# Kernel tuning notes

Hardware: AMD Instinct MI355X
Metric: run time of the kernel (lower is better)

## Reference

```python
import jax, jax.numpy as jnp
import numpy as np

B, S, D = 4, 512, 512


def setup_inputs() -> dict:
    key = jax.random.key(0)
    k0, k1, k2 = jax.random.split(key, 3)
    x = jax.random.normal(k0, (B, S, D), jnp.float32)
    W1 = jax.random.normal(k1, (D, D // 2), jnp.float32) / np.sqrt(D).astype(np.float32)
    b1 = jnp.zeros((D // 2,), jnp.float32)
    W2 = jax.random.normal(k2, (D // 2, 1), jnp.float32) / np.sqrt(D // 2).astype(np.float32)
    b2 = jnp.zeros((1,), jnp.float32)
    # deterministic ragged durations in the module's ~10-30 frame range
    durations = jnp.broadcast_to(8 + (jnp.arange(S, dtype=jnp.int32) % 32), (B, S))
    total_length = int(np.asarray(durations).sum())  # 48128, static
    return dict(x=x, W1=W1, b1=b1, W2=W2, b2=b2, durations=durations,
                total_length=total_length)


def reference(x, W1, b1, W2, b2, durations, total_length):
    # --- duration-predictor MLP (Linear -> ReLU -> Linear -> Softplus) ---
    h = jax.nn.relu(jnp.einsum('bsd,df->bsf', x, W1) + b1)
    dur_mlp = jax.nn.softplus(jnp.einsum('bsf,fo->bso', h, W2) + b2)[..., 0]  # [B,S]

    # --- length regulation: gather + linear interpolation ---
    # torch code uses durations of batch row 0 for all batch elements, and
    # allocates total_length = sum over the WHOLE batch (trailing zeros kept).
    dur0 = durations[0].astype(jnp.int32)          # [S]
    csum = jnp.cumsum(dur0)                         # [S], csum[-1] = used length L
    L = csum[-1]
    t = jnp.arange(total_length, dtype=jnp.int32)   # [T]
    tok = jnp.searchsorted(csum, t, side='right')   # token index per output frame
    valid = t < L
    ic = jnp.minimum(tok, S - 1)
    j = t - (csum[ic] - dur0[ic])                   # offset within token's frames
    # last token: pure repeat (alpha=0); others: lerp toward x[:, i+1]
    alpha = jnp.where(ic == S - 1, 0.0,
                      j.astype(x.dtype) / dur0[ic].astype(x.dtype))  # [T]
    left = x[:, ic]                                 # [B,T,D]
    right = x[:, jnp.minimum(ic + 1, S - 1)]        # [B,T,D]
    a = alpha[None, :, None]
    expanded = (1.0 - a) * left + a * right
    expanded = jnp.where(valid[None, :, None], expanded, 0.0)
    return expanded, dur_mlp
```

## Files before the change

kernel.cpp:

```cpp
#include <hip/hip_runtime.h>
#include <math.h>

#define Bn 4
#define Sn 512
#define Dn 512
#define Fn 256
#define RROWS 8

struct Ent { float alpha; int ic; };

typedef float v4f __attribute__((ext_vector_type(4)));

__global__ __launch_bounds__(512) void prep_kernel(const int* __restrict__ dur,
                                                   Ent* __restrict__ tab, int T) {
    __shared__ int csum[Sn];
    int tid = threadIdx.x;
    csum[tid] = dur[tid];
    __syncthreads();
    #pragma unroll
    for (int off = 1; off < Sn; off <<= 1) {
        int add = (tid >= off) ? csum[tid - off] : 0;
        __syncthreads();
        csum[tid] += add;
        __syncthreads();
    }
    int L = csum[Sn - 1];
    int t = blockIdx.x * Sn + tid;
    if (t >= T) return;
    Ent e;
    if (t >= L) {
        e.alpha = 0.f; e.ic = -1;
    } else {
        int lo = 0, hi = Sn;
        while (lo < hi) {
            int mid = (lo + hi) >> 1;
            if (csum[mid] <= t) lo = mid + 1; else hi = mid;
        }
        int ic = lo;
        int start = ic ? csum[ic - 1] : 0;
        int d = csum[ic] - start;
        e.ic = ic;
        e.alpha = (ic == Sn - 1) ? 0.f : (float)(t - start) / (float)d;
    }
    tab[t] = e;
}

__global__ __launch_bounds__(256) void mlp_kernel(const float* __restrict__ x,
                                                  const float* __restrict__ W1,
                                                  const float* __restrict__ b1,
                                                  const float* __restrict__ W2,
                                                  const float* __restrict__ b2,
                                                  float* __restrict__ out_dur) {
    __shared__ float xs[RROWS][Dn];
    __shared__ float red[4][RROWS];
    int f = threadIdx.x;
    int r0 = blockIdx.x * RROWS;

    const float4* src = (const float4*)(x + (size_t)r0 * Dn);
    float4* dst = (float4*)(&xs[0][0]);
    for (int i = f; i < RROWS * Dn / 4; i += 256) dst[i] = src[i];
    __syncthreads();

    float acc[RROWS];
    #pragma unroll
    for (int r = 0; r < RROWS; r++) acc[r] = 0.f;

    for (int k = 0; k < Dn; k += 4) {
        float w0 = W1[(k + 0) * Fn + f];
        float w1 = W1[(k + 1) * Fn + f];
        float w2 = W1[(k + 2) * Fn + f];
        float w3 = W1[(k + 3) * Fn + f];
        #pragma unroll
        for (int r = 0; r < RROWS; r++) {
            float4 xv = *(const float4*)&xs[r][k];
            acc[r] += xv.x * w0 + xv.y * w1 + xv.z * w2 + xv.w * w3;
        }
    }

    float bb = b1[f], wf = W2[f];
    float p[RROWS];
    #pragma unroll
    for (int r = 0; r < RROWS; r++) {
        float h = acc[r] + bb;
        h = h > 0.f ? h : 0.f;
        p[r] = h * wf;
    }

    int lane = f & 63, wv = f >> 6;
    #pragma unroll
    for (int r = 0; r < RROWS; r++) {
        float v = p[r];
        #pragma unroll
        for (int off = 32; off > 0; off >>= 1) v += __shfl_down(v, off, 64);
        if (lane == 0) red[wv][r] = v;
    }
    __syncthreads();
    if (f < RROWS) {
        float z = red[0][f] + red[1][f] + red[2][f] + red[3][f] + b2[0];
        float sp = fmaxf(z, 0.f) + log1pf(expf(-fabsf(z)));
        out_dur[r0 + f] = sp;
    }
}

__global__ __launch_bounds__(256) void expand_kernel(const float* __restrict__ x,
                                                     const Ent* __restrict__ tab,
                                                     float* __restrict__ out, int T) {
    int idx = blockIdx.x * 256 + threadIdx.x;
    int total = T << 7;
    if (idx >= total) return;
    int b = blockIdx.y;
    int t = idx >> 7;
    int d4 = idx & 127;

    Ent e = tab[t];
    float4 res;
    if (e.ic < 0) {
        res = make_float4(0.f, 0.f, 0.f, 0.f);
    } else {
        const float* xb = x + (size_t)b * (Sn * Dn);
        int icr = e.ic + 1; if (icr > Sn - 1) icr = Sn - 1;
        float4 l = ((const float4*)(xb + (size_t)e.ic * Dn))[d4];
        float4 r = ((const float4*)(xb + (size_t)icr * Dn))[d4];
        float a = e.alpha, na = 1.f - a;
        res.x = na * l.x + a * r.x;
        res.y = na * l.y + a * r.y;
        res.z = na * l.z + a * r.z;
        res.w = na * l.w + a * r.w;
    }
    float4* op = (float4*)(out + ((size_t)b * T + t) * Dn) + d4;
    __builtin_nontemporal_store(*(const v4f*)&res, (v4f*)op);
}

extern "C" void kernel_launch(void* const* d_in, const int* in_sizes, int n_in,
                              void* d_out, int out_size, void* d_ws, size_t ws_size,
                              hipStream_t stream) {
    const float* x   = (const float*)d_in[0];
    const float* W1  = (const float*)d_in[1];
    const float* b1  = (const float*)d_in[2];
    const float* W2  = (const float*)d_in[3];
    const float* b2  = (const float*)d_in[4];
    const int* durs  = (const int*)d_in[5];
    float* out = (float*)d_out;

    int T = (out_size - Bn * Sn) / (Bn * Dn);
    Ent* tab = (Ent*)d_ws;

    dim3 pgrid((T + Sn - 1) / Sn);
    prep_kernel<<<pgrid, Sn, 0, stream>>>(durs, tab, T);

    float* dur_out = out + ((size_t)out_size - Bn * Sn);
    mlp_kernel<<<dim3((Bn * Sn) / RROWS), 256, 0, stream>>>(x, W1, b1, W2, b2, dur_out);

    int total4 = T * (Dn / 4);
    dim3 egrid((total4 + 255) / 256, Bn);
    expand_kernel<<<egrid, 256, 0, stream>>>(x, tab, out, T);
}
```

Measured before the change: 426.7 us.

## Fuse MLP and expand kernels into one launch with split-K and batch loop

Merges the duration MLP and the length-regulation expand into a single kernel. The first blocks run the MLP with 512 threads, splitting the K dimension in half and combining the partial sums through shared memory. The remaining blocks handle the expand, with each thread looping over all four batches and covering two float4 columns, so each table entry is read once and more loads are in flight per thread. This removes one launch and lets the compute-bound MLP overlap the bandwidth-bound expand. The cost is larger blocks, more shared memory, and more registers per thread.

```diff
diff --git a/kernel.cpp b/kernel.cpp
--- a/kernel.cpp
+++ b/kernel.cpp
@@ -6,6 +6,7 @@
 #define Dn 512
 #define Fn 256
 #define RROWS 8
+#define MLPB ((Bn * Sn) / RROWS)
 
 struct Ent { float alpha; int ic; };
 
@@ -45,90 +46,115 @@
     tab[t] = e;
 }
 
-__global__ __launch_bounds__(256) void mlp_kernel(const float* __restrict__ x,
-                                                  const float* __restrict__ W1,
-                                                  const float* __restrict__ b1,
-                                                  const float* __restrict__ W2,
-                                                  const float* __restrict__ b2,
-                                                  float* __restrict__ out_dur) {
+__global__ __launch_bounds__(512) void fused_kernel(const float* __restrict__ x,
+                                                    const float* __restrict__ W1,
+                                                    const float* __restrict__ b1,
+                                                    const float* __restrict__ W2,
+                                                    const float* __restrict__ b2,
+                                                    const Ent* __restrict__ tab,
+                                                    float* __restrict__ out,
+                                                    float* __restrict__ dur_out,
+                                                    int T) {
     __shared__ float xs[RROWS][Dn];
+    __shared__ float ps[RROWS][256];
     __shared__ float red[4][RROWS];
-    int f = threadIdx.x;
-    int r0 = blockIdx.x * RROWS;
 
-    const float4* src = (const float4*)(x + (size_t)r0 * Dn);
-    float4* dst = (float4*)(&xs[0][0]);
-    for (int i = f; i < RROWS * Dn / 4; i += 256) dst[i] = src[i];
-    __syncthreads();
+    if (blockIdx.x < MLPB) {
+        int tid = threadIdx.x;
+        int f = tid & 255;
+        int half = tid >> 8;
+        int r0 = blockIdx.x * RROWS;
 
-    float acc[RROWS];
-    #pragma unroll
-    for (int r = 0; r < RROWS; r++) acc[r] = 0.f;
+        const float4* src = (const float4*)(x + (size_t)r0 * Dn);
+        float4* dst = (float4*)(&xs[0][0]);
+        dst[tid] = src[tid];
+        dst[tid + 512] = src[tid + 512];
+        __syncthreads();
 
-    for (int k = 0; k < Dn; k += 4) {
-        float w0 = W1[(k + 0) * Fn + f];
-        float w1 = W1[(k + 1) * Fn + f];
-        float w2 = W1[(k + 2) * Fn + f];
-        float w3 = W1[(k + 3) * Fn + f];
+        float acc[RROWS];
         #pragma unroll
-        for (int r = 0; r < RROWS; r++) {
-            float4 xv = *(const float4*)&xs[r][k];
-            acc[r] += xv.x * w0 + xv.y * w1 + xv.z * w2 + xv.w * w3;
+        for (int r = 0; r < RROWS; r++) acc[r] = 0.f;
+
+        int kbeg = half * (Dn / 2);
+        for (int k = kbeg; k < kbeg + Dn / 2; k += 4) {
+            float w0 = W1[(k + 0) * Fn + f];
+            float w1 = W1[(k + 1) * Fn + f];
+            float w2 = W1[(k + 2) * Fn + f];
+            float w3 = W1[(k + 3) * Fn + f];
+            #pragma unroll
+            for (int r = 0; r < RROWS; r++) {
+                float4 xv = *(const float4*)&xs[r][k];
+                acc[r] += xv.x * w0 + xv.y * w1 + xv.z * w2 + xv.w * w3;
+            }
+        }
+
+        if (half) {
+            #pragma unroll
+            for (int r = 0; r < RROWS; r++) ps[r][f] = acc[r];
+        }
+        __syncthreads();
+
+        if (!half) {
+            float bb = b1[f], wf = W2[f];
+            int lane = f & 63, wv = f >> 6;
+            #pragma unroll
+            for (int r = 0; r < RROWS; r++) {
+                float h = acc[r] + ps[r][f] + bb;
+                h = h > 0.f ? h : 0.f;
+                float v = h * wf;
+                #pragma unroll
+                for (int off = 32; off > 0; off >>= 1) v += __shfl_down(v, off, 64);
+                if (lane == 0) red[wv][r] = v;
+            }
+        }
+        __syncthreads();
+        if (threadIdx.x < RROWS) {
+            int r = threadIdx.x;
+            float z = red[0][r] + red[1][r] + red[2][r] + red[3][r] + b2[0];
+            float sp = fmaxf(z, 0.f) + log1pf(expf(-fabsf(z)));
+            dur_out[r0 + r] = sp;
+        }
+        return;
+    }
+
+    int idx = (blockIdx.x - MLPB) * 512 + threadIdx.x;
+    if (idx >= (T << 6)) return;
+    int t = idx >> 6;
+    int d4 = idx & 63;
+
+    Ent e = tab[t];
+    if (e.ic < 0) {
+        v4f z = {0.f, 0.f, 0.f, 0.f};
+        #pragma unroll
+        for (int b = 0; b < Bn; b++) {
+            float* op = out + ((size_t)b * T + t) * Dn;
+            __builtin_nontemporal_store(z, (v4f*)op + d4);
+            __builtin_nontemporal_store(z, (v4f*)op + d4 + 64);
+        }
+    } else {
+        int icr = e.ic + 1; if (icr > Sn - 1) icr = Sn - 1;
+        float a = e.alpha, na = 1.f - a;
+        #pragma unroll
+        for (int b = 0; b < Bn; b++) {
+            const float* xb = x + (size_t)b * (Sn * Dn);
+            const float4* lp = (const float4*)(xb + (size_t)e.ic * Dn);
+            const float4* rp = (const float4*)(xb + (size_t)icr * Dn);
+            float4 l0 = lp[d4],      r0 = rp[d4];
+            float4 l1 = lp[d4 + 64], r1 = rp[d4 + 64];
+            v4f o0, o1;
+            o0.x = na * l0.x + a * r0.x;
+            o0.y = na * l0.y + a * r0.y;
+            o0.z = na * l0.z + a * r0.z;
+            o0.w = na * l0.w + a * r0.w;
+            o1.x = na * l1.x + a * r1.x;
+            o1.y = na * l1.y + a * r1.y;
+            o1.z = na * l1.z + a * r1.z;
+            o1.w = na * l1.w + a * r1.w;
+            float* op = out + ((size_t)b * T + t) * Dn;
+            __builtin_nontemporal_store(o0, (v4f*)op + d4);
+            __builtin_nontemporal_store(o1, (v4f*)op + d4 + 64);
         }
     }
-
-    float bb = b1[f], wf = W2[f];
-    float p[RROWS];
-    #pragma unroll
-    for (int r = 0; r < RROWS; r++) {
-        float h = acc[r] + bb;
-        h = h > 0.f ? h : 0.f;
-        p[r] = h * wf;
-    }
-
-    int lane = f & 63, wv = f >> 6;
-    #pragma unroll
-    for (int r = 0; r < RROWS; r++) {
-        float v = p[r];
-        #pragma unroll
-        for (int off = 32; off > 0; off >>= 1) v += __shfl_down(v, off, 64);
-        if (lane == 0) red[wv][r] = v;
-    }
-    __syncthreads();
-    if (f < RROWS) {
-        float z = red[0][f] + red[1][f] + red[2][f] + red[3][f] + b2[0];
-        float sp = fmaxf(z, 0.f) + log1pf(expf(-fabsf(z)));
-        out_dur[r0 + f] = sp;
-    }
-}
-
-__global__ __launch_bounds__(256) void expand_kernel(const float* __restrict__ x,
-                                                     const Ent* __restrict__ tab,
-                                                     float* __restrict__ out, int T) {
-    int idx = blockIdx.x * 256 + threadIdx.x;
-    int total = T << 7;
-    if (idx >= total) return;
-    int b = blockIdx.y;
-    int t = idx >> 7;
-    int d4 = idx & 127;
-
-    Ent e = tab[t];
-    float4 res;
-    if (e.ic < 0) {
-        res = make_float4(0.f, 0.f, 0.f, 0.f);
-    } else {
-        const float* xb = x + (size_t)b * (Sn * Dn);
-        int icr = e.ic + 1; if (icr > Sn - 1) icr = Sn - 1;
-        float4 l = ((const float4*)(xb + (size_t)e.ic * Dn))[d4];
-        float4 r = ((const float4*)(xb + (size_t)icr * Dn))[d4];
-        float a = e.alpha, na = 1.f - a;
-        res.x = na * l.x + a * r.x;
-        res.y = na * l.y + a * r.y;
-        res.z = na * l.z + a * r.z;
-        res.w = na * l.w + a * r.w;
-    }
-    float4* op = (float4*)(out + ((size_t)b * T + t) * Dn) + d4;
-    __builtin_nontemporal_store(*(const v4f*)&res, (v4f*)op);
 }
 
 extern "C" void kernel_launch(void* const* d_in, const int* in_sizes, int n_in,
@@ -149,9 +175,7 @@
     prep_kernel<<<pgrid, Sn, 0, stream>>>(durs, tab, T);
 
     float* dur_out = out + ((size_t)out_size - Bn * Sn);
-    mlp_kernel<<<dim3((Bn * Sn) / RROWS), 256, 0, stream>>>(x, W1, b1, W2, b2, dur_out);
-
-    int total4 = T * (Dn / 4);
-    dim3 egrid((total4 + 255) / 256, Bn);
-    expand_kernel<<<egrid, 256, 0, stream>>>(x, tab, out, T);
+    int eblk = ((T << 6) + 511) / 512;
+    fused_kernel<<<MLPB + eblk, 512, 0, stream>>>(x, W1, b1, W2, b2, tab, out,
+                                                  dur_out, T);
 }
```

Measured after the change: 427.0 us. Within noise of the previous version (+0.1%).
